# Performance work log

Hardware: AMD Instinct MI355X
Metric: run time of the kernel (lower is better)

Reference implementation:

```python
import jax, jax.numpy as jnp
import numpy as np

KERNEL_SIZE = 7
STRIDE = 1
PADDING = 3
DILATION = 1


def setup_inputs() -> dict:
    key = jax.random.key(0)
    x = jax.random.normal(key, (8, 64, 56, 56), dtype=jnp.float32)
    return {"x": x}


def reference(x):
    """Pairwise subtraction (SAN): center pixel minus each of its k*k
    dilated neighbors, zero-padded borders (pad_mode=0).
    Output: [n, c, k*k, out_h*out_w]."""
    k, s, p, d = KERNEL_SIZE, STRIDE, PADDING, DILATION
    n, c, H, W = x.shape
    out_h = (H + 2 * p - (d * (k - 1) + 1)) // s + 1
    out_w = (W + 2 * p - (d * (k - 1) + 1)) // s + 1
    # centers: unfold with kernel 1, no padding, stride s
    centers = x[:, :, ::s, ::s][:, :, :out_h, :out_w]  # n,c,out_h,out_w
    # neighbors: zero-pad then take k*k strided slices (row-major kernel order
    # to match nn.Unfold)
    xp = jnp.pad(x, ((0, 0), (0, 0), (p, p), (p, p)))
    patches = jnp.stack(
        [
            xp[:, :, i * d : i * d + s * (out_h - 1) + 1 : s,
                     j * d : j * d + s * (out_w - 1) + 1 : s]
            for i in range(k)
            for j in range(k)
        ],
        axis=2,
    )  # n, c, k*k, out_h, out_w
    out = centers.reshape(n, c, 1, out_h * out_w) - patches.reshape(
        n, c, k * k, out_h * out_w
    )
    return out
```

## Files before the change

### kernel.cpp

```cpp
#include <hip/hip_runtime.h>


constexpr int N_ = 8, C_ = 64, H_ = 56, W_ = 56;
constexpr int K_ = 7, P_ = 3;
constexpr int KK_  = K_ * K_;
constexpr int OHW_ = H_ * W_;
constexpr int O4_  = W_ / 4;
constexpr int POS4_ = N_ * C_ * H_ * O4_;

typedef float f32x4 __attribute__((ext_vector_type(4)));

__global__ __launch_bounds__(256)
void san_kernel(const float* __restrict__ x, float* __restrict__ out) {
    int idx = blockIdx.x * 256 + threadIdx.x;

    int o4 = idx % O4_;
    int t1 = idx / O4_;
    int oh = t1 % H_;
    int nc = t1 / H_;
    int ow = o4 * 4;

    const float* plane = x + (size_t)nc * OHW_;

    float win[K_][12];
    #pragma unroll
    for (int di = 0; di < K_; ++di) {
        int r = oh + di - P_;
        bool rv = (unsigned)r < (unsigned)H_;
        #pragma unroll
        for (int q = 0; q < 3; ++q) {
            int c = ow + 4 * q - 4;
            f32x4 v = {0.f, 0.f, 0.f, 0.f};
            if (rv && (unsigned)c < (unsigned)W_) {
                v = *reinterpret_cast<const f32x4*>(plane + r * W_ + c);
            }
            win[di][4 * q + 0] = v[0];
            win[di][4 * q + 1] = v[1];
            win[di][4 * q + 2] = v[2];
            win[di][4 * q + 3] = v[3];
        }
    }

    float cen0 = win[P_][4], cen1 = win[P_][5], cen2 = win[P_][6], cen3 = win[P_][7];

    float* op = out + (size_t)nc * KK_ * OHW_ + oh * W_ + ow;

    #pragma unroll
    for (int ki = 0; ki < K_; ++ki) {
        #pragma unroll
        for (int kj = 0; kj < K_; ++kj) {
            f32x4 res;
            res[0] = cen0 - win[ki][kj + 1];
            res[1] = cen1 - win[ki][kj + 2];
            res[2] = cen2 - win[ki][kj + 3];
            res[3] = cen3 - win[ki][kj + 4];
            *reinterpret_cast<f32x4*>(op) = res;
            op += OHW_;
        }
    }
}

extern "C" void kernel_launch(void* const* d_in, const int* in_sizes, int n_in,
                              void* d_out, int out_size, void* d_ws, size_t ws_size,
                              hipStream_t stream) {
    const float* x = (const float*)d_in[0];
    float* out = (float*)d_out;
    san_kernel<<<POS4_ / 256, 256, 0, stream>>>(x, out);
}
```

Baseline: 59.09 us.

## Stage each channel plane in zero-padded LDS and compute neighbors from shared memory

Each block now handles one full (n,c) plane. It loads the plane once into a zero-padded LDS tile and reads every neighbor window from LDS instead of issuing many overlapping global loads per thread. This removes redundant global and L2 reads and the per-load bounds checks. The cost is fewer, larger blocks (512), an LDS zeroing pass and syncs, and a load imbalance: only 16 threads do a fourth chunk of serial stores. The kernel is bound by output writes, so the effect may be small.

After: 57.44 us (median of 2 runs). -2.8%, faster.

```diff
diff --git a/kernel.cpp b/kernel.cpp
--- a/kernel.cpp
+++ b/kernel.cpp
@@ -1,61 +1,86 @@
 #include <hip/hip_runtime.h>
 
 
-constexpr int N_ = 8, C_ = 64, H_ = 56, W_ = 56;
-constexpr int K_ = 7, P_ = 3;
-constexpr int KK_  = K_ * K_;
-constexpr int OHW_ = H_ * W_;
-constexpr int O4_  = W_ / 4;
-constexpr int POS4_ = N_ * C_ * H_ * O4_;
+constexpr int H_ = 56, W_ = 56;
+constexpr int KK_  = 49;
+constexpr int OHW_ = 3136;
+constexpr int PP_  = 63;
+constexpr int PR_  = 62;
+constexpr int NC_  = 512;
+constexpr int LDSN_ = PR_ * PP_;
 
 typedef float f32x4 __attribute__((ext_vector_type(4)));
 
 __global__ __launch_bounds__(256)
 void san_kernel(const float* __restrict__ x, float* __restrict__ out) {
-    int idx = blockIdx.x * 256 + threadIdx.x;
+    __shared__ float lds[LDSN_];
+    const int nc = blockIdx.x;
+    const int t  = threadIdx.x;
 
-    int o4 = idx % O4_;
-    int t1 = idx / O4_;
-    int oh = t1 % H_;
-    int nc = t1 / H_;
-    int ow = o4 * 4;
+    #pragma unroll
+    for (int i = 0; i < 16; ++i) {
+        int j = t + 256 * i;
+        if (j < LDSN_) lds[j] = 0.0f;
+    }
+    __syncthreads();
 
     const float* plane = x + (size_t)nc * OHW_;
 
-    float win[K_][12];
+    f32x4 cen0{}, cen1{}, cen2{}, cen3{};
+    int ab0 = 0, ab1 = 0, ab2 = 0, ab3 = 0;
+    const bool has3 = (t < 16);
+
+#define STAGE(S, CEN, AB)                                           \
+    {                                                               \
+        int e4 = t + 256 * (S);                                     \
+        int oh = e4 / 14, o4 = e4 - oh * 14;                        \
+        CEN = *reinterpret_cast<const f32x4*>(plane + e4 * 4);      \
+        int lb = (oh + 3) * PP_ + o4 * 4 + 3;                       \
+        lds[lb + 0] = CEN[0]; lds[lb + 1] = CEN[1];                 \
+        lds[lb + 2] = CEN[2]; lds[lb + 3] = CEN[3];                 \
+        AB = oh * PP_ + o4 * 4;                                     \
+    }
+    STAGE(0, cen0, ab0)
+    STAGE(1, cen1, ab1)
+    STAGE(2, cen2, ab2)
+    if (has3) STAGE(3, cen3, ab3)
+#undef STAGE
+    __syncthreads();
+
+    float* ob  = out + (size_t)nc * (KK_ * OHW_);
+    float* op0 = ob + (size_t)(t      ) * 4;
+    float* op1 = ob + (size_t)(t + 256) * 4;
+    float* op2 = ob + (size_t)(t + 512) * 4;
+
     #pragma unroll
-    for (int di = 0; di < K_; ++di) {
-        int r = oh + di - P_;
-        bool rv = (unsigned)r < (unsigned)H_;
+    for (int ki = 0; ki < 7; ++ki) {
         #pragma unroll
-        for (int q = 0; q < 3; ++q) {
-            int c = ow + 4 * q - 4;
-            f32x4 v = {0.f, 0.f, 0.f, 0.f};
-            if (rv && (unsigned)c < (unsigned)W_) {
-                v = *reinterpret_cast<const f32x4*>(plane + r * W_ + c);
+        for (int kj = 0; kj < 7; ++kj) {
+            const int off = ki * PP_ + kj;
+            f32x4 r0, r1, r2;
+            #pragma unroll
+            for (int tt = 0; tt < 4; ++tt) {
+                r0[tt] = cen0[tt] - lds[ab0 + off + tt];
+                r1[tt] = cen1[tt] - lds[ab1 + off + tt];
+                r2[tt] = cen2[tt] - lds[ab2 + off + tt];
             }
-            win[di][4 * q + 0] = v[0];
-            win[di][4 * q + 1] = v[1];
-            win[di][4 * q + 2] = v[2];
-            win[di][4 * q + 3] = v[3];
+            *reinterpret_cast<f32x4*>(op0) = r0;  op0 += OHW_;
+            *reinterpret_cast<f32x4*>(op1) = r1;  op1 += OHW_;
+            *reinterpret_cast<f32x4*>(op2) = r2;  op2 += OHW_;
         }
     }
 
-    float cen0 = win[P_][4], cen1 = win[P_][5], cen2 = win[P_][6], cen3 = win[P_][7];
-
-    float* op = out + (size_t)nc * KK_ * OHW_ + oh * W_ + ow;
-
-    #pragma unroll
-    for (int ki = 0; ki < K_; ++ki) {
-        #pragma unroll
-        for (int kj = 0; kj < K_; ++kj) {
-            f32x4 res;
-            res[0] = cen0 - win[ki][kj + 1];
-            res[1] = cen1 - win[ki][kj + 2];
-            res[2] = cen2 - win[ki][kj + 3];
-            res[3] = cen3 - win[ki][kj + 4];
-            *reinterpret_cast<f32x4*>(op) = res;
-            op += OHW_;
+    if (has3) {
+        float* op3 = ob + (size_t)(t + 768) * 4;
+        for (int ki = 0; ki < 7; ++ki) {
+            for (int kj = 0; kj < 7; ++kj) {
+                int off = ki * PP_ + kj;
+                f32x4 r;
+                #pragma unroll
+                for (int tt = 0; tt < 4; ++tt)
+                    r[tt] = cen3[tt] - lds[ab3 + off + tt];
+                *reinterpret_cast<f32x4*>(op3) = r;  op3 += OHW_;
+            }
         }
     }
 }
@@ -65,5 +90,5 @@
                               hipStream_t stream) {
     const float* x = (const float*)d_in[0];
     float* out = (float*)d_out;
-    san_kernel<<<POS4_ / 256, 256, 0, stream>>>(x, out);
+    san_kernel<<<NC_, 256, 0, stream>>>(x, out);
 }
```
